# Kernel tuning notes

Measured on AMD Instinct MI355X. Metric: run time of the kernel, lower is better.

Reference implementation:

```python
import jax, jax.numpy as jnp
import numpy as np

D_MODEL = 1024
NUM_HEADS = 16
D_HEAD = D_MODEL // NUM_HEADS


def rotate_half(x):
    half = x.shape[-1] // 2
    x1, x2 = x[..., :half], x[..., half:]
    return jnp.concatenate((-x2, x1), axis=-1)


def rope_cos_sin(seq_len, d_head, dtype):
    # inv_freq over even dims of d_head
    inv_freq = 1.0 / (10000.0 ** (jnp.arange(0, d_head, 2, dtype=jnp.float32) / d_head))
    t = jnp.arange(seq_len, dtype=jnp.float32)
    freqs = jnp.einsum('i,j->ij', t, inv_freq)        # [L, d_head/2]
    emb = jnp.concatenate((freqs, freqs), axis=-1)    # [L, d_head]
    return jnp.cos(emb).astype(dtype), jnp.sin(emb).astype(dtype)


def setup_inputs() -> dict:
    key = jax.random.key(0)
    ks = jax.random.split(key, 9)
    B, L = 2, 2048
    s = 1.0 / np.sqrt(D_MODEL)
    return {
        'x': jax.random.normal(ks[0], (B, L, D_MODEL), dtype=jnp.float32),
        'Wq': jax.random.normal(ks[1], (D_MODEL, D_MODEL), dtype=jnp.float32) * s,
        'bq': jax.random.normal(ks[2], (D_MODEL,), dtype=jnp.float32) * 0.02,
        'Wk': jax.random.normal(ks[3], (D_MODEL, D_MODEL), dtype=jnp.float32) * s,
        'bk': jax.random.normal(ks[4], (D_MODEL,), dtype=jnp.float32) * 0.02,
        'Wv': jax.random.normal(ks[5], (D_MODEL, D_MODEL), dtype=jnp.float32) * s,
        'bv': jax.random.normal(ks[6], (D_MODEL,), dtype=jnp.float32) * 0.02,
        'Wo': jax.random.normal(ks[7], (D_MODEL, D_MODEL), dtype=jnp.float32) * s,
        'bo': jax.random.normal(ks[8], (D_MODEL,), dtype=jnp.float32) * 0.02,
    }


def reference(x, Wq, bq, Wk, bk, Wv, bv, Wo, bo):
    B, L, D = x.shape
    H, Dh = NUM_HEADS, D_HEAD
    scale = Dh ** -0.5

    # projections: torch Linear is x @ W.T + b; here W stored as [in, out]-like
    # square matrices, so treat Wq etc. directly as x @ Wq + bq.
    q = (x @ Wq + bq).reshape(B, L, H, Dh).transpose(0, 2, 1, 3)  # [B,H,L,Dh]
    k = (x @ Wk + bk).reshape(B, L, H, Dh).transpose(0, 2, 1, 3)
    v = (x @ Wv + bv).reshape(B, L, H, Dh).transpose(0, 2, 1, 3)

    cos, sin = rope_cos_sin(L, Dh, x.dtype)  # [L, Dh]
    cos = cos[None, None]  # [1,1,L,Dh]
    sin = sin[None, None]
    q = q * cos + rotate_half(q) * sin
    k = k * cos + rotate_half(k) * sin

    attn = jnp.einsum('bhqd,bhkd->bhqk', q, k) * scale  # [B,H,L,L]
    attn = jax.nn.softmax(attn, axis=-1)
    out = jnp.einsum('bhqk,bhkd->bhqd', attn, v)        # [B,H,L,Dh]
    out = out.transpose(0, 2, 1, 3).reshape(B, L, D)
    return out @ Wo + bo
```

## Files before the change

kernel.cpp:

```cpp
#include <hip/hip_runtime.h>
#include <cmath>

#define D_MODEL  1024
#define NHEADS   16
#define DHEAD    64
#define BATCH    2
#define SEQ      2048
#define MROWS    (BATCH * SEQ)
#define HALF_DH  32

typedef __attribute__((ext_vector_type(8))) short short8;
typedef __attribute__((ext_vector_type(4))) float f32x4;
typedef __attribute__((ext_vector_type(16))) float f32x16;

#define MFMA16(A,B,C) __builtin_amdgcn_mfma_f32_16x16x32_bf16(A,B,C,0,0,0)
#define MFMA32(A,B,C) __builtin_amdgcn_mfma_f32_32x32x16_bf16(A,B,C,0,0,0)

__device__ __forceinline__ unsigned short f2bf(float f) {
    unsigned int u = __float_as_uint(f);
    u += 0x7fffu + ((u >> 16) & 1u);
    return (unsigned short)(u >> 16);
}

__device__ __forceinline__ void gload_lds16(const void* g, void* l) {
    __builtin_amdgcn_global_load_lds(
        (const __attribute__((address_space(1))) unsigned int*)g,
        (__attribute__((address_space(3))) unsigned int*)l,
        16, 0, 0);
}

__global__ void rope_table_kernel(float* __restrict__ cosT, float* __restrict__ sinT) {
    int idx = blockIdx.x * blockDim.x + threadIdx.x;
    if (idx >= SEQ * HALF_DH) return;
    int l = idx >> 5;
    int j = idx & 31;
    float inv = powf(10000.0f, -(float)(2 * j) / (float)DHEAD);
    float ang = (float)l * inv;
    cosT[idx] = cosf(ang);
    sinT[idx] = sinf(ang);
}

__global__ __launch_bounds__(256)
void convert_bf16_kernel(const float* __restrict__ in, unsigned short* __restrict__ out) {
    int i = blockIdx.x * 256 + threadIdx.x;
    float4 v = ((const float4*)in)[i];
    ushort4 o;
    o.x = f2bf(v.x); o.y = f2bf(v.y); o.z = f2bf(v.z); o.w = f2bf(v.w);
    ((ushort4*)out)[i] = o;
}

__global__ __launch_bounds__(256)
void wtrans_kernel(const float* __restrict__ W, unsigned short* __restrict__ Wt) {
    __shared__ unsigned short T[64][68];
    const int k0 = blockIdx.x * 64, n0 = blockIdx.y * 64;
    const int t = threadIdx.x, r = t >> 4, cq = t & 15;
    #pragma unroll
    for (int p = 0; p < 4; ++p) {
        int k = r + 16 * p;
        float4 v = *(const float4*)&W[(size_t)(k0 + k) * D_MODEL + n0 + cq * 4];
        T[cq * 4 + 0][k] = f2bf(v.x);
        T[cq * 4 + 1][k] = f2bf(v.y);
        T[cq * 4 + 2][k] = f2bf(v.z);
        T[cq * 4 + 3][k] = f2bf(v.w);
    }
    __syncthreads();
    #pragma unroll
    for (int p = 0; p < 4; ++p) {
        int n = r + 16 * p;
        ushort4 o;
        o.x = T[n][cq * 4 + 0]; o.y = T[n][cq * 4 + 1];
        o.z = T[n][cq * 4 + 2]; o.w = T[n][cq * 4 + 3];
        *(ushort4*)&Wt[(size_t)(n0 + n) * D_MODEL + k0 + cq * 4] = o;
    }
}

template<int MODE>
__global__ __launch_bounds__(256)
void proj_mfma_kernel(const unsigned short* __restrict__ A, const unsigned short* __restrict__ Bt,
                      const float* __restrict__ bias, const float* __restrict__ cosT,
                      const float* __restrict__ sinT, void* __restrict__ outp)
{
    __shared__ unsigned short As[128 * 64];
    __shared__ unsigned short Bs[64 * 64];
    const int tid = threadIdx.x;
    const int w = tid >> 6, ln = tid & 63;
    const int c = ln & 15, g = ln >> 4;
    const int bm = blockIdx.x * 128, bn = blockIdx.y * 64;
    const int srow = ln >> 3, sblk = ln & 7;

    f32x4 acc[2][4];
    #pragma unroll
    for (int mi = 0; mi < 2; ++mi)
        #pragma unroll
        for (int ni = 0; ni < 4; ++ni) acc[mi][ni] = (f32x4){0.f, 0.f, 0.f, 0.f};

    for (int k0 = 0; k0 < D_MODEL; k0 += 64) {
        __syncthreads();
        #pragma unroll
        for (int i = 0; i < 4; ++i) {
            int chunk = w * 4 + i;
            int row = chunk * 8 + srow;
            int gcol = (sblk ^ (row & 7)) * 8;
            gload_lds16(&A[(size_t)(bm + row) * D_MODEL + k0 + gcol], &As[chunk * 512]);
        }
        #pragma unroll
        for (int i = 0; i < 2; ++i) {
            int chunk = w * 2 + i;
            int row = chunk * 8 + srow;
            int gcol = (sblk ^ (row & 7)) * 8;
            gload_lds16(&Bt[(size_t)(bn + row) * D_MODEL + k0 + gcol], &Bs[chunk * 512]);
        }
        __syncthreads();

        #pragma unroll
        for (int ks = 0; ks < 2; ++ks) {
            const int koff = (ks * 32 + g * 8) ^ ((c & 7) * 8);
            short8 af[2];
            #pragma unroll
            for (int mi = 0; mi < 2; ++mi)
                af[mi] = *(const short8*)&As[(w * 32 + mi * 16 + c) * 64 + koff];
            #pragma unroll
            for (int ni = 0; ni < 4; ++ni) {
                short8 bfr = *(const short8*)&Bs[(ni * 16 + c) * 64 + koff];
                #pragma unroll
                for (int mi = 0; mi < 2; ++mi)
                    acc[mi][ni] = MFMA16(af[mi], bfr, acc[mi][ni]);
            }
        }
    }

    float bv[4];
    #pragma unroll
    for (int ni = 0; ni < 4; ++ni) bv[ni] = bias[bn + ni * 16 + c];

    #pragma unroll
    for (int mi = 0; mi < 2; ++mi) {
        #pragma unroll
        for (int r = 0; r < 4; ++r) {
            const int m = bm + w * 32 + mi * 16 + g * 4 + r;
            float v[4];
            #pragma unroll
            for (int ni = 0; ni < 4; ++ni) v[ni] = acc[mi][ni][r] + bv[ni];
            if (MODE == 2) {
                float* out = (float*)outp;
                #pragma unroll
                for (int ni = 0; ni < 4; ++ni)
                    out[(size_t)m * D_MODEL + bn + ni * 16 + c] = v[ni];
            } else {
                const int b = m >> 11, ll = m & (SEQ - 1);
                if (MODE == 0) {
                    #pragma unroll
                    for (int ni = 0; ni < 2; ++ni) {
                        int d = ni * 16 + c;
                        float co = cosT[ll * HALF_DH + d];
                        float si = sinT[ll * HALF_DH + d];
                        float lo = v[ni], hi = v[ni + 2];
                        v[ni]     = lo * co - hi * si;
                        v[ni + 2] = hi * co + lo * si;
                    }
                }
                const int h = blockIdx.y;
                unsigned short* dst = (unsigned short*)outp
                    + ((size_t)(b * NHEADS + h) * SEQ + ll) * DHEAD;
                #pragma unroll
                for (int ni = 0; ni < 4; ++ni) dst[ni * 16 + c] = f2bf(v[ni]);
            }
        }
    }
}

__global__ __launch_bounds__(256)
void vtrans_kernel(const unsigned short* __restrict__ V, unsigned short* __restrict__ Vt) {
    __shared__ unsigned short T[64][68];
    const int bh = blockIdx.y, l0 = blockIdx.x * 64;
    const int t = threadIdx.x, r = t >> 4, cq = t & 15;
    const unsigned short* Vb = V + (size_t)bh * SEQ * DHEAD;
    #pragma unroll
    for (int p = 0; p < 4; ++p) {
        int ll = r + 16 * p;
        ushort4 v = *(const ushort4*)&Vb[(size_t)(l0 + ll) * DHEAD + cq * 4];
        T[cq * 4 + 0][ll] = v.x; T[cq * 4 + 1][ll] = v.y;
        T[cq * 4 + 2][ll] = v.z; T[cq * 4 + 3][ll] = v.w;
    }
    __syncthreads();
    unsigned short* Vo = Vt + (size_t)bh * DHEAD * SEQ;
    #pragma unroll
    for (int p = 0; p < 4; ++p) {
        int d = r + 16 * p;
        ushort4 o;
        o.x = T[d][cq * 4 + 0]; o.y = T[d][cq * 4 + 1];
        o.z = T[d][cq * 4 + 2]; o.w = T[d][cq * 4 + 3];
        *(ushort4*)&Vo[(size_t)d * SEQ + l0 + cq * 4] = o;
    }
}

__global__ __launch_bounds__(256, 2)
void attn_mfma32_kernel(const unsigned short* __restrict__ Q, const unsigned short* __restrict__ K,
                        const unsigned short* __restrict__ Vt, unsigned short* __restrict__ O)
{
    __shared__ unsigned short Ks[2][64 * 64];
    __shared__ unsigned short Vs[2][64 * 64];
    const int tid = threadIdx.x;
    const int w = tid >> 6, ln = tid & 63;
    const int ql = ln & 31;
    const int h  = ln >> 5;
    const int bh = blockIdx.y;
    const int q  = blockIdx.x * 128 + w * 32 + ql;
    const float SC = 0.125f * 1.44269504088896340736f;
    const int srow = ln >> 3, sblk = ln & 7;

    const unsigned short* Qb = Q  + (size_t)bh * SEQ * DHEAD;
    const unsigned short* Kb = K  + (size_t)bh * SEQ * DHEAD;
    const unsigned short* Vb = Vt + (size_t)bh * DHEAD * SEQ;

    short8 qf[4];
    #pragma unroll
    for (int dk = 0; dk < 4; ++dk)
        qf[dk] = *(const short8*)&Qb[(size_t)q * DHEAD + dk * 16 + h * 8];

    f32x16 accO0, accO1;
    #pragma unroll
    for (int r = 0; r < 16; ++r) { accO0[r] = 0.f; accO1[r] = 0.f; }
    float accL = 0.f, mst = -1e30f;

    #pragma unroll
    for (int i = 0; i < 2; ++i) {
        int chunk = w * 2 + i;
        int row = chunk * 8 + srow;
        int gcol = (sblk ^ (row & 7)) * 8;
        gload_lds16(&Kb[(size_t)row * DHEAD + gcol], &Ks[0][chunk * 512]);
        gload_lds16(&Vb[(size_t)row * SEQ + gcol],   &Vs[0][chunk * 512]);
    }
    __syncthreads();

    int cur = 0;
    for (int kt = 0; kt < SEQ; kt += 64) {
        if (kt + 64 < SEQ) {
            #pragma unroll
            for (int i = 0; i < 2; ++i) {
                int chunk = w * 2 + i;
                int row = chunk * 8 + srow;
                int gcol = (sblk ^ (row & 7)) * 8;
                gload_lds16(&Kb[(size_t)(kt + 64 + row) * DHEAD + gcol], &Ks[cur ^ 1][chunk * 512]);
                gload_lds16(&Vb[(size_t)row * SEQ + kt + 64 + gcol],     &Vs[cur ^ 1][chunk * 512]);
            }
        }

        f32x16 s0, s1;
        #pragma unroll
        for (int r = 0; r < 16; ++r) { s0[r] = 0.f; s1[r] = 0.f; }
        #pragma unroll
        for (int dk = 0; dk < 4; ++dk) {
            const int off = ((2 * dk + h) ^ (ql & 7)) * 8;
            short8 kf0 = *(const short8*)&Ks[cur][ql * 64 + off];
            short8 kf1 = *(const short8*)&Ks[cur][(32 + ql) * 64 + off];
            s0 = MFMA32(kf0, qf[dk], s0);
            s1 = MFMA32(kf1, qf[dk], s1);
        }

        float mx = s0[0];
        #pragma unroll
        for (int r = 1; r < 16; ++r) mx = fmaxf(mx, s0[r]);
        #pragma unroll
        for (int r = 0; r < 16; ++r) mx = fmaxf(mx, s1[r]);
        mx = fmaxf(mx, __shfl_xor(mx, 32));
        const float mn = fmaxf(mst, mx);
        const float rsc = exp2f((mst - mn) * SC);
        mst = mn;

        #pragma unroll
        for (int r = 0; r < 16; ++r) {
            s0[r] = exp2f((s0[r] - mn) * SC);
            s1[r] = exp2f((s1[r] - mn) * SC);
        }

        float ts = 0.f;
        #pragma unroll
        for (int r = 0; r < 16; ++r) ts += s0[r] + s1[r];
        ts += __shfl_xor(ts, 32);
        accL = accL * rsc + ts;

        #pragma unroll
        for (int r = 0; r < 16; ++r) { accO0[r] *= rsc; accO1[r] *= rsc; }

        short8 pf[4];
        #define REPACK_T(T, SV)                                                          \
        {                                                                                \
            unsigned int wA0, wA1, wB0, wB1;                                             \
            asm("v_cvt_pk_bf16_f32 %0, %1, %2" : "=v"(wA0)                               \
                : "v"((SV)[8 * ((T) & 1) + 0]), "v"((SV)[8 * ((T) & 1) + 1]));           \
            asm("v_cvt_pk_bf16_f32 %0, %1, %2" : "=v"(wA1)                               \
                : "v"((SV)[8 * ((T) & 1) + 2]), "v"((SV)[8 * ((T) & 1) + 3]));           \
            asm("v_cvt_pk_bf16_f32 %0, %1, %2" : "=v"(wB0)                               \
                : "v"((SV)[8 * ((T) & 1) + 4]), "v"((SV)[8 * ((T) & 1) + 5]));           \
            asm("v_cvt_pk_bf16_f32 %0, %1, %2" : "=v"(wB1)                               \
                : "v"((SV)[8 * ((T) & 1) + 6]), "v"((SV)[8 * ((T) & 1) + 7]));           \
            asm("v_permlane32_swap_b32 %0, %1" : "+v"(wA0), "+v"(wB0));                  \
            asm("v_permlane32_swap_b32 %0, %1" : "+v"(wA1), "+v"(wB1));                  \
            union { short8 v; unsigned int u[4]; } tmp;                                  \
            tmp.u[0] = wA0; tmp.u[1] = wA1; tmp.u[2] = wB0; tmp.u[3] = wB1;              \
            pf[T] = tmp.v;                                                               \
        }
        REPACK_T(0, s0) REPACK_T(1, s0) REPACK_T(2, s1) REPACK_T(3, s1)
        #undef REPACK_T

        #pragma unroll
        for (int t = 0; t < 4; ++t) {
            const int off = ((2 * t + h) ^ (ql & 7)) * 8;
            short8 vf0 = *(const short8*)&Vs[cur][ql * 64 + off];
            short8 vf1 = *(const short8*)&Vs[cur][(32 + ql) * 64 + off];
            accO0 = MFMA32(vf0, pf[t], accO0);
            accO1 = MFMA32(vf1, pf[t], accO1);
        }

        __syncthreads();
        cur ^= 1;
    }

    const int b = bh >> 4, hh = bh & 15;
    const float inv = 1.0f / accL;
    unsigned short* dst = O + ((size_t)(b * SEQ + q)) * D_MODEL + hh * DHEAD;
    #define EPI(ACC, DC)                                                                 \
    {                                                                                    \
        _Pragma("unroll")                                                                \
        for (int rq = 0; rq < 4; ++rq) {                                                 \
            float a0 = (ACC)[4 * rq + 0] * inv, a1 = (ACC)[4 * rq + 1] * inv;            \
            float a2 = (ACC)[4 * rq + 2] * inv, a3 = (ACC)[4 * rq + 3] * inv;            \
            unsigned int p0, p1;                                                         \
            asm("v_cvt_pk_bf16_f32 %0, %1, %2" : "=v"(p0) : "v"(a0), "v"(a1));           \
            asm("v_cvt_pk_bf16_f32 %0, %1, %2" : "=v"(p1) : "v"(a2), "v"(a3));           \
            uint2 pk; pk.x = p0; pk.y = p1;                                              \
            *(uint2*)(dst + 32 * (DC) + 8 * rq + 4 * h) = pk;                            \
        }                                                                                \
    }
    EPI(accO0, 0) EPI(accO1, 1)
    #undef EPI
}

extern "C" void kernel_launch(void* const* d_in, const int* in_sizes, int n_in,
                              void* d_out, int out_size, void* d_ws, size_t ws_size,
                              hipStream_t stream)
{
    const float* x  = (const float*)d_in[0];
    const float* Wq = (const float*)d_in[1];
    const float* bq = (const float*)d_in[2];
    const float* Wk = (const float*)d_in[3];
    const float* bk = (const float*)d_in[4];
    const float* Wv = (const float*)d_in[5];
    const float* bv = (const float*)d_in[6];
    const float* Wo = (const float*)d_in[7];
    const float* bo = (const float*)d_in[8];

    float* cosT = (float*)d_ws;
    float* sinT = cosT + SEQ * HALF_DH;
    unsigned short* xb  = (unsigned short*)(sinT + SEQ * HALF_DH);
    unsigned short* wqT = xb  + (size_t)MROWS * D_MODEL;
    unsigned short* wkT = wqT + (size_t)D_MODEL * D_MODEL;
    unsigned short* wvT = wkT + (size_t)D_MODEL * D_MODEL;
    unsigned short* woT = wvT + (size_t)D_MODEL * D_MODEL;
    unsigned short* qb  = woT + (size_t)D_MODEL * D_MODEL;
    unsigned short* kb  = qb  + (size_t)MROWS * D_MODEL;
    unsigned short* vb  = kb  + (size_t)MROWS * D_MODEL;
    unsigned short* vtb = vb  + (size_t)MROWS * D_MODEL;
    unsigned short* ob  = vtb + (size_t)MROWS * D_MODEL;

    rope_table_kernel<<<(SEQ * HALF_DH + 255) / 256, 256, 0, stream>>>(cosT, sinT);
    convert_bf16_kernel<<<(MROWS * D_MODEL / 4) / 256, 256, 0, stream>>>(x, xb);

    dim3 wgrid(D_MODEL / 64, D_MODEL / 64);
    wtrans_kernel<<<wgrid, 256, 0, stream>>>(Wq, wqT);
    wtrans_kernel<<<wgrid, 256, 0, stream>>>(Wk, wkT);
    wtrans_kernel<<<wgrid, 256, 0, stream>>>(Wv, wvT);
    wtrans_kernel<<<wgrid, 256, 0, stream>>>(Wo, woT);

    dim3 pgrid(MROWS / 128, D_MODEL / 64);
    proj_mfma_kernel<0><<<pgrid, 256, 0, stream>>>(xb, wqT, bq, cosT, sinT, qb);
    proj_mfma_kernel<0><<<pgrid, 256, 0, stream>>>(xb, wkT, bk, cosT, sinT, kb);
    proj_mfma_kernel<1><<<pgrid, 256, 0, stream>>>(xb, wvT, bv, cosT, sinT, vb);

    dim3 vgrid(SEQ / 64, BATCH * NHEADS);
    vtrans_kernel<<<vgrid, 256, 0, stream>>>(vb, vtb);

    dim3 agrid(SEQ / 128, BATCH * NHEADS);
    attn_mfma32_kernel<<<agrid, 256, 0, stream>>>(qb, kb, vtb, ob);

    proj_mfma_kernel<2><<<pgrid, 256, 0, stream>>>(ob, woT, bo, cosT, sinT, d_out);
}
```

Baseline: 168.5 us.

## Fuse QKV projections with V transpose, split-K attention, lazy softmax rescale

Merges the four weight-transpose launches into one and the three QKV projection launches into one grid-z kernel. The V projection now writes its transposed layout directly through LDS, which removes the separate vtrans pass. Attention is split along the key dimension into two halves to double the grid, with a combine kernel merging the partial results. The online softmax now skips rescaling when the running max does not change, uses tree reductions, and raises the occupancy hint. This costs extra fp32 partial-result traffic and an additional launch for the combine step.

```diff
diff --git a/kernel.cpp b/kernel.cpp
--- a/kernel.cpp
+++ b/kernel.cpp
@@ -8,6 +8,8 @@
 #define SEQ      2048
 #define MROWS    (BATCH * SEQ)
 #define HALF_DH  32
+#define BHTOT    (BATCH * NHEADS)
+#define QROWS    (BHTOT * SEQ)
 
 typedef __attribute__((ext_vector_type(8))) short short8;
 typedef __attribute__((ext_vector_type(4))) float f32x4;
@@ -50,35 +52,164 @@
 }
 
 __global__ __launch_bounds__(256)
-void wtrans_kernel(const float* __restrict__ W, unsigned short* __restrict__ Wt) {
+void wtrans4_kernel(const float* __restrict__ Wq, const float* __restrict__ Wk,
+                    const float* __restrict__ Wv, const float* __restrict__ Wo,
+                    unsigned short* __restrict__ q, unsigned short* __restrict__ k,
+                    unsigned short* __restrict__ v, unsigned short* __restrict__ o)
+{
     __shared__ unsigned short T[64][68];
+    const float* W; unsigned short* Wt;
+    switch (blockIdx.z) {
+        case 0:  W = Wq; Wt = q; break;
+        case 1:  W = Wk; Wt = k; break;
+        case 2:  W = Wv; Wt = v; break;
+        default: W = Wo; Wt = o; break;
+    }
     const int k0 = blockIdx.x * 64, n0 = blockIdx.y * 64;
     const int t = threadIdx.x, r = t >> 4, cq = t & 15;
     #pragma unroll
     for (int p = 0; p < 4; ++p) {
-        int k = r + 16 * p;
-        float4 v = *(const float4*)&W[(size_t)(k0 + k) * D_MODEL + n0 + cq * 4];
-        T[cq * 4 + 0][k] = f2bf(v.x);
-        T[cq * 4 + 1][k] = f2bf(v.y);
-        T[cq * 4 + 2][k] = f2bf(v.z);
-        T[cq * 4 + 3][k] = f2bf(v.w);
+        int kk = r + 16 * p;
+        float4 vv = *(const float4*)&W[(size_t)(k0 + kk) * D_MODEL + n0 + cq * 4];
+        T[cq * 4 + 0][kk] = f2bf(vv.x);
+        T[cq * 4 + 1][kk] = f2bf(vv.y);
+        T[cq * 4 + 2][kk] = f2bf(vv.z);
+        T[cq * 4 + 3][kk] = f2bf(vv.w);
     }
     __syncthreads();
     #pragma unroll
     for (int p = 0; p < 4; ++p) {
         int n = r + 16 * p;
-        ushort4 o;
-        o.x = T[n][cq * 4 + 0]; o.y = T[n][cq * 4 + 1];
-        o.z = T[n][cq * 4 + 2]; o.w = T[n][cq * 4 + 3];
-        *(ushort4*)&Wt[(size_t)(n0 + n) * D_MODEL + k0 + cq * 4] = o;
-    }
-}
-
-template<int MODE>
+        ushort4 ov;
+        ov.x = T[n][cq * 4 + 0]; ov.y = T[n][cq * 4 + 1];
+        ov.z = T[n][cq * 4 + 2]; ov.w = T[n][cq * 4 + 3];
+        *(ushort4*)&Wt[(size_t)(n0 + n) * D_MODEL + k0 + cq * 4] = ov;
+    }
+}
+
 __global__ __launch_bounds__(256)
-void proj_mfma_kernel(const unsigned short* __restrict__ A, const unsigned short* __restrict__ Bt,
-                      const float* __restrict__ bias, const float* __restrict__ cosT,
-                      const float* __restrict__ sinT, void* __restrict__ outp)
+void qkv_proj_kernel(const unsigned short* __restrict__ A,
+                     const unsigned short* __restrict__ wqT, const unsigned short* __restrict__ wkT,
+                     const unsigned short* __restrict__ wvT,
+                     const float* __restrict__ bq, const float* __restrict__ bk,
+                     const float* __restrict__ bv,
+                     const float* __restrict__ cosT, const float* __restrict__ sinT,
+                     unsigned short* __restrict__ qb, unsigned short* __restrict__ kb,
+                     unsigned short* __restrict__ vtb)
+{
+    __shared__ unsigned short SMEM[128 * 64 + 64 * 64];
+    unsigned short* As = SMEM;
+    unsigned short* Bs = SMEM + 128 * 64;
+
+    const int z = blockIdx.z;
+    const unsigned short* Bt = (z == 0) ? wqT : (z == 1) ? wkT : wvT;
+    const float* bias = (z == 0) ? bq : (z == 1) ? bk : bv;
+
+    const int tid = threadIdx.x;
+    const int w = tid >> 6, ln = tid & 63;
+    const int c = ln & 15, g = ln >> 4;
+    const int bm = blockIdx.x * 128, bn = blockIdx.y * 64;
+    const int srow = ln >> 3, sblk = ln & 7;
+
+    f32x4 acc[2][4];
+    #pragma unroll
+    for (int mi = 0; mi < 2; ++mi)
+        #pragma unroll
+        for (int ni = 0; ni < 4; ++ni) acc[mi][ni] = (f32x4){0.f, 0.f, 0.f, 0.f};
+
+    for (int k0 = 0; k0 < D_MODEL; k0 += 64) {
+        __syncthreads();
+        #pragma unroll
+        for (int i = 0; i < 4; ++i) {
+            int chunk = w * 4 + i;
+            int row = chunk * 8 + srow;
+            int gcol = (sblk ^ (row & 7)) * 8;
+            gload_lds16(&A[(size_t)(bm + row) * D_MODEL + k0 + gcol], &As[chunk * 512]);
+        }
+        #pragma unroll
+        for (int i = 0; i < 2; ++i) {
+            int chunk = w * 2 + i;
+            int row = chunk * 8 + srow;
+            int gcol = (sblk ^ (row & 7)) * 8;
+            gload_lds16(&Bt[(size_t)(bn + row) * D_MODEL + k0 + gcol], &Bs[chunk * 512]);
+        }
+        __syncthreads();
+
+        #pragma unroll
+        for (int ks = 0; ks < 2; ++ks) {
+            const int koff = (ks * 32 + g * 8) ^ ((c & 7) * 8);
+            short8 af[2];
+            #pragma unroll
+            for (int mi = 0; mi < 2; ++mi)
+                af[mi] = *(const short8*)&As[(w * 32 + mi * 16 + c) * 64 + koff];
+            #pragma unroll
+            for (int ni = 0; ni < 4; ++ni) {
+                short8 bfr = *(const short8*)&Bs[(ni * 16 + c) * 64 + koff];
+                #pragma unroll
+                for (int mi = 0; mi < 2; ++mi)
+                    acc[mi][ni] = MFMA16(af[mi], bfr, acc[mi][ni]);
+            }
+        }
+    }
+
+    float bv4[4];
+    #pragma unroll
+    for (int ni = 0; ni < 4; ++ni) bv4[ni] = bias[bn + ni * 16 + c];
+
+    if (z < 2) {
+        unsigned short* op = z ? kb : qb;
+        const int hy = blockIdx.y;
+        #pragma unroll
+        for (int mi = 0; mi < 2; ++mi) {
+            #pragma unroll
+            for (int r = 0; r < 4; ++r) {
+                const int m = bm + w * 32 + mi * 16 + g * 4 + r;
+                const int b = m >> 11, ll = m & (SEQ - 1);
+                float v[4];
+                #pragma unroll
+                for (int ni = 0; ni < 4; ++ni) v[ni] = acc[mi][ni][r] + bv4[ni];
+                #pragma unroll
+                for (int ni = 0; ni < 2; ++ni) {
+                    int d = ni * 16 + c;
+                    float co = cosT[ll * HALF_DH + d];
+                    float si = sinT[ll * HALF_DH + d];
+                    float lo = v[ni], hi = v[ni + 2];
+                    v[ni]     = lo * co - hi * si;
+                    v[ni + 2] = hi * co + lo * si;
+                }
+                unsigned short* dst = op + ((size_t)(b * NHEADS + hy) * SEQ + ll) * DHEAD;
+                #pragma unroll
+                for (int ni = 0; ni < 4; ++ni) dst[ni * 16 + c] = f2bf(v[ni]);
+            }
+        }
+    } else {
+        unsigned short (*T)[136] = (unsigned short(*)[136])SMEM;
+        __syncthreads();
+        #pragma unroll
+        for (int mi = 0; mi < 2; ++mi)
+            #pragma unroll
+            for (int r = 0; r < 4; ++r)
+                #pragma unroll
+                for (int ni = 0; ni < 4; ++ni)
+                    T[ni * 16 + c][w * 32 + mi * 16 + g * 4 + r] = f2bf(acc[mi][ni][r] + bv4[ni]);
+        __syncthreads();
+        const int b  = bm >> 11;
+        const int l0 = bm & (SEQ - 1);
+        const int bh = b * NHEADS + blockIdx.y;
+        unsigned short* Vo = vtb + (size_t)bh * DHEAD * SEQ;
+        #pragma unroll
+        for (int it = 0; it < 4; ++it) {
+            int row  = (tid >> 4) + it * 16;
+            int col8 = tid & 15;
+            uint4 val = *(const uint4*)&T[row][col8 * 8];
+            *(uint4*)&Vo[(size_t)row * SEQ + l0 + col8 * 8] = val;
+        }
+    }
+}
+
+__global__ __launch_bounds__(256)
+void outproj_kernel(const unsigned short* __restrict__ A, const unsigned short* __restrict__ Bt,
+                    const float* __restrict__ bias, float* __restrict__ out)
 {
     __shared__ unsigned short As[128 * 64];
     __shared__ unsigned short Bs[64 * 64];
@@ -129,74 +260,24 @@
         }
     }
 
-    float bv[4];
-    #pragma unroll
-    for (int ni = 0; ni < 4; ++ni) bv[ni] = bias[bn + ni * 16 + c];
-
-    #pragma unroll
-    for (int mi = 0; mi < 2; ++mi) {
+    float bv4[4];
+    #pragma unroll
+    for (int ni = 0; ni < 4; ++ni) bv4[ni] = bias[bn + ni * 16 + c];
+    #pragma unroll
+    for (int mi = 0; mi < 2; ++mi)
         #pragma unroll
         for (int r = 0; r < 4; ++r) {
             const int m = bm + w * 32 + mi * 16 + g * 4 + r;
-            float v[4];
-            #pragma unroll
-            for (int ni = 0; ni < 4; ++ni) v[ni] = acc[mi][ni][r] + bv[ni];
-            if (MODE == 2) {
-                float* out = (float*)outp;
-                #pragma unroll
-                for (int ni = 0; ni < 4; ++ni)
-                    out[(size_t)m * D_MODEL + bn + ni * 16 + c] = v[ni];
-            } else {
-                const int b = m >> 11, ll = m & (SEQ - 1);
-                if (MODE == 0) {
-                    #pragma unroll
-                    for (int ni = 0; ni < 2; ++ni) {
-                        int d = ni * 16 + c;
-                        float co = cosT[ll * HALF_DH + d];
-                        float si = sinT[ll * HALF_DH + d];
-                        float lo = v[ni], hi = v[ni + 2];
-                        v[ni]     = lo * co - hi * si;
-                        v[ni + 2] = hi * co + lo * si;
-                    }
-                }
-                const int h = blockIdx.y;
-                unsigned short* dst = (unsigned short*)outp
-                    + ((size_t)(b * NHEADS + h) * SEQ + ll) * DHEAD;
-                #pragma unroll
-                for (int ni = 0; ni < 4; ++ni) dst[ni * 16 + c] = f2bf(v[ni]);
-            }
-        }
-    }
-}
-
-__global__ __launch_bounds__(256)
-void vtrans_kernel(const unsigned short* __restrict__ V, unsigned short* __restrict__ Vt) {
-    __shared__ unsigned short T[64][68];
-    const int bh = blockIdx.y, l0 = blockIdx.x * 64;
-    const int t = threadIdx.x, r = t >> 4, cq = t & 15;
-    const unsigned short* Vb = V + (size_t)bh * SEQ * DHEAD;
-    #pragma unroll
-    for (int p = 0; p < 4; ++p) {
-        int ll = r + 16 * p;
-        ushort4 v = *(const ushort4*)&Vb[(size_t)(l0 + ll) * DHEAD + cq * 4];
-        T[cq * 4 + 0][ll] = v.x; T[cq * 4 + 1][ll] = v.y;
-        T[cq * 4 + 2][ll] = v.z; T[cq * 4 + 3][ll] = v.w;
-    }
-    __syncthreads();
-    unsigned short* Vo = Vt + (size_t)bh * DHEAD * SEQ;
-    #pragma unroll
-    for (int p = 0; p < 4; ++p) {
-        int d = r + 16 * p;
-        ushort4 o;
-        o.x = T[d][cq * 4 + 0]; o.y = T[d][cq * 4 + 1];
-        o.z = T[d][cq * 4 + 2]; o.w = T[d][cq * 4 + 3];
-        *(ushort4*)&Vo[(size_t)d * SEQ + l0 + cq * 4] = o;
-    }
-}
-
-__global__ __launch_bounds__(256, 2)
+            #pragma unroll
+            for (int ni = 0; ni < 4; ++ni)
+                out[(size_t)m * D_MODEL + bn + ni * 16 + c] = acc[mi][ni][r] + bv4[ni];
+        }
+}
+
+__global__ __launch_bounds__(256, 4)
 void attn_mfma32_kernel(const unsigned short* __restrict__ Q, const unsigned short* __restrict__ K,
-                        const unsigned short* __restrict__ Vt, unsigned short* __restrict__ O)
+                        const unsigned short* __restrict__ Vt, unsigned short* __restrict__ O,
+                        float* __restrict__ accP, float* __restrict__ ml, int nsplit)
 {
     __shared__ unsigned short Ks[2][64 * 64];
     __shared__ unsigned short Vs[2][64 * 64];
@@ -206,6 +287,9 @@
     const int h  = ln >> 5;
     const int bh = blockIdx.y;
     const int q  = blockIdx.x * 128 + w * 32 + ql;
+    const int split = blockIdx.z;
+    const int ntile = SEQ / (64 * nsplit);
+    const int kt0 = split * (SEQ / nsplit);
     const float SC = 0.125f * 1.44269504088896340736f;
     const int srow = ln >> 3, sblk = ln & 7;
 
@@ -228,14 +312,15 @@
         int chunk = w * 2 + i;
         int row = chunk * 8 + srow;
         int gcol = (sblk ^ (row & 7)) * 8;
-        gload_lds16(&Kb[(size_t)row * DHEAD + gcol], &Ks[0][chunk * 512]);
-        gload_lds16(&Vb[(size_t)row * SEQ + gcol],   &Vs[0][chunk * 512]);
+        gload_lds16(&Kb[(size_t)(kt0 + row) * DHEAD + gcol], &Ks[0][chunk * 512]);
+        gload_lds16(&Vb[(size_t)row * SEQ + kt0 + gcol],     &Vs[0][chunk * 512]);
     }
     __syncthreads();
 
     int cur = 0;
-    for (int kt = 0; kt < SEQ; kt += 64) {
-        if (kt + 64 < SEQ) {
+    for (int it = 0; it < ntile; ++it) {
+        const int kt = kt0 + it * 64;
+        if (it + 1 < ntile) {
             #pragma unroll
             for (int i = 0; i < 2; ++i) {
                 int chunk = w * 2 + i;
@@ -258,30 +343,41 @@
             s1 = MFMA32(kf1, qf[dk], s1);
         }
 
-        float mx = s0[0];
-        #pragma unroll
-        for (int r = 1; r < 16; ++r) mx = fmaxf(mx, s0[r]);
-        #pragma unroll
-        for (int r = 0; r < 16; ++r) mx = fmaxf(mx, s1[r]);
+        float m16[16];
+        #pragma unroll
+        for (int r = 0; r < 16; ++r) m16[r] = fmaxf(s0[r], s1[r]);
+        #pragma unroll
+        for (int st = 8; st >= 1; st >>= 1)
+            #pragma unroll
+            for (int r = 0; r < st; ++r) m16[r] = fmaxf(m16[r], m16[r + st]);
+        float mx = m16[0];
         mx = fmaxf(mx, __shfl_xor(mx, 32));
+
         const float mn = fmaxf(mst, mx);
-        const float rsc = exp2f((mst - mn) * SC);
-        mst = mn;
+        if (__any(mn > mst)) {
+            const float rsc = exp2f((mst - mn) * SC);
+            #pragma unroll
+            for (int r = 0; r < 16; ++r) { accO0[r] *= rsc; accO1[r] *= rsc; }
+            accL *= rsc;
+            mst = mn;
+        }
 
         #pragma unroll
         for (int r = 0; r < 16; ++r) {
-            s0[r] = exp2f((s0[r] - mn) * SC);
-            s1[r] = exp2f((s1[r] - mn) * SC);
-        }
-
-        float ts = 0.f;
-        #pragma unroll
-        for (int r = 0; r < 16; ++r) ts += s0[r] + s1[r];
+            s0[r] = exp2f((s0[r] - mst) * SC);
+            s1[r] = exp2f((s1[r] - mst) * SC);
+        }
+
+        float t16[16];
+        #pragma unroll
+        for (int r = 0; r < 16; ++r) t16[r] = s0[r] + s1[r];
+        #pragma unroll
+        for (int st = 8; st >= 1; st >>= 1)
+            #pragma unroll
+            for (int r = 0; r < st; ++r) t16[r] += t16[r + st];
+        float ts = t16[0];
         ts += __shfl_xor(ts, 32);
-        accL = accL * rsc + ts;
-
-        #pragma unroll
-        for (int r = 0; r < 16; ++r) { accO0[r] *= rsc; accO1[r] *= rsc; }
+        accL += ts;
 
         short8 pf[4];
         #define REPACK_T(T, SV)                                                          \
@@ -317,24 +413,70 @@
         cur ^= 1;
     }
 
-    const int b = bh >> 4, hh = bh & 15;
-    const float inv = 1.0f / accL;
-    unsigned short* dst = O + ((size_t)(b * SEQ + q)) * D_MODEL + hh * DHEAD;
-    #define EPI(ACC, DC)                                                                 \
-    {                                                                                    \
-        _Pragma("unroll")                                                                \
-        for (int rq = 0; rq < 4; ++rq) {                                                 \
-            float a0 = (ACC)[4 * rq + 0] * inv, a1 = (ACC)[4 * rq + 1] * inv;            \
-            float a2 = (ACC)[4 * rq + 2] * inv, a3 = (ACC)[4 * rq + 3] * inv;            \
-            unsigned int p0, p1;                                                         \
-            asm("v_cvt_pk_bf16_f32 %0, %1, %2" : "=v"(p0) : "v"(a0), "v"(a1));           \
-            asm("v_cvt_pk_bf16_f32 %0, %1, %2" : "=v"(p1) : "v"(a2), "v"(a3));           \
-            uint2 pk; pk.x = p0; pk.y = p1;                                              \
-            *(uint2*)(dst + 32 * (DC) + 8 * rq + 4 * h) = pk;                            \
-        }                                                                                \
-    }
-    EPI(accO0, 0) EPI(accO1, 1)
-    #undef EPI
+    if (nsplit == 1) {
+        const int b = bh >> 4, hh = bh & 15;
+        const float inv = 1.0f / accL;
+        unsigned short* dst = O + ((size_t)(b * SEQ + q)) * D_MODEL + hh * DHEAD;
+        #define EPI(ACC, DC)                                                             \
+        {                                                                                \
+            _Pragma("unroll")                                                            \
+            for (int rq = 0; rq < 4; ++rq) {                                             \
+                float a0 = (ACC)[4 * rq + 0] * inv, a1 = (ACC)[4 * rq + 1] * inv;        \
+                float a2 = (ACC)[4 * rq + 2] * inv, a3 = (ACC)[4 * rq + 3] * inv;        \
+                unsigned int p0, p1;                                                     \
+                asm("v_cvt_pk_bf16_f32 %0, %1, %2" : "=v"(p0) : "v"(a0), "v"(a1));       \
+                asm("v_cvt_pk_bf16_f32 %0, %1, %2" : "=v"(p1) : "v"(a2), "v"(a3));       \
+                uint2 pk; pk.x = p0; pk.y = p1;                                          \
+                *(uint2*)(dst + 32 * (DC) + 8 * rq + 4 * h) = pk;                        \
+            }                                                                            \
+        }
+        EPI(accO0, 0) EPI(accO1, 1)
+        #undef EPI
+    } else {
+        float* base = accP + ((size_t)(split * BHTOT + bh) * SEQ + q) * 64;
+        #pragma unroll
+        for (int rq = 0; rq < 4; ++rq) {
+            float4 v0, v1;
+            v0.x = accO0[4 * rq + 0]; v0.y = accO0[4 * rq + 1];
+            v0.z = accO0[4 * rq + 2]; v0.w = accO0[4 * rq + 3];
+            v1.x = accO1[4 * rq + 0]; v1.y = accO1[4 * rq + 1];
+            v1.z = accO1[4 * rq + 2]; v1.w = accO1[4 * rq + 3];
+            *(float4*)&base[8 * rq + 4 * h]      = v0;
+            *(float4*)&base[32 + 8 * rq + 4 * h] = v1;
+        }
+        if (h == 0) {
+            float2 v; v.x = mst; v.y = accL;
+            ((float2*)ml)[(size_t)(split * BHTOT + bh) * SEQ + q] = v;
+        }
+    }
+}
+
+__global__ __launch_bounds__(256)
+void combine2_kernel(const float* __restrict__ accP, const float* __restrict__ ml,
+                     unsigned short* __restrict__ ob)
+{
+    const float SC = 0.125f * 1.44269504088896340736f;
+    int t = blockIdx.x * 256 + threadIdx.x;
+    int d4  = (t & 15) * 4;
+    int bhq = t >> 4;
+    const float2* ML = (const float2*)ml;
+    float2 m0 = ML[bhq];
+    float2 m1 = ML[(size_t)QROWS + bhq];
+    float M  = fmaxf(m0.x, m1.x);
+    float w0 = exp2f((m0.x - M) * SC);
+    float w1 = exp2f((m1.x - M) * SC);
+    float inv = 1.0f / (w0 * m0.y + w1 * m1.y);
+    float4 a0 = *(const float4*)&accP[(size_t)bhq * 64 + d4];
+    float4 a1 = *(const float4*)&accP[(size_t)QROWS * 64 + (size_t)bhq * 64 + d4];
+    float o0 = (a0.x * w0 + a1.x * w1) * inv;
+    float o1 = (a0.y * w0 + a1.y * w1) * inv;
+    float o2 = (a0.z * w0 + a1.z * w1) * inv;
+    float o3 = (a0.w * w0 + a1.w * w1) * inv;
+    int bh = bhq >> 11, q = bhq & (SEQ - 1);
+    int b = bh >> 4, hh = bh & 15;
+    ushort4 ov;
+    ov.x = f2bf(o0); ov.y = f2bf(o1); ov.z = f2bf(o2); ov.w = f2bf(o3);
+    *(ushort4*)&ob[((size_t)(b * SEQ + q)) * D_MODEL + hh * DHEAD + d4] = ov;
 }
 
 extern "C" void kernel_launch(void* const* d_in, const int* in_sizes, int n_in,
@@ -351,38 +493,37 @@
     const float* Wo = (const float*)d_in[7];
     const float* bo = (const float*)d_in[8];
 
-    float* cosT = (float*)d_ws;
-    float* sinT = cosT + SEQ * HALF_DH;
-    unsigned short* xb  = (unsigned short*)(sinT + SEQ * HALF_DH);
-    unsigned short* wqT = xb  + (size_t)MROWS * D_MODEL;
-    unsigned short* wkT = wqT + (size_t)D_MODEL * D_MODEL;
-    unsigned short* wvT = wkT + (size_t)D_MODEL * D_MODEL;
-    unsigned short* woT = wvT + (size_t)D_MODEL * D_MODEL;
-    unsigned short* qb  = woT + (size_t)D_MODEL * D_MODEL;
-    unsigned short* kb  = qb  + (size_t)MROWS * D_MODEL;
-    unsigned short* vb  = kb  + (size_t)MROWS * D_MODEL;
-    unsigned short* vtb = vb  + (size_t)MROWS * D_MODEL;
-    unsigned short* ob  = vtb + (size_t)MROWS * D_MODEL;
+    char* p = (char*)d_ws;
+    float* cosT = (float*)p;            p += (size_t)SEQ * HALF_DH * 4;
+    float* sinT = (float*)p;            p += (size_t)SEQ * HALF_DH * 4;
+    unsigned short* xb  = (unsigned short*)p; p += (size_t)MROWS * D_MODEL * 2;
+    unsigned short* wqT = (unsigned short*)p; p += (size_t)D_MODEL * D_MODEL * 2;
+    unsigned short* wkT = (unsigned short*)p; p += (size_t)D_MODEL * D_MODEL * 2;
+    unsigned short* wvT = (unsigned short*)p; p += (size_t)D_MODEL * D_MODEL * 2;
+    unsigned short* woT = (unsigned short*)p; p += (size_t)D_MODEL * D_MODEL * 2;
+    unsigned short* qb  = (unsigned short*)p; p += (size_t)MROWS * D_MODEL * 2;
+    unsigned short* kb  = (unsigned short*)p; p += (size_t)MROWS * D_MODEL * 2;
+    unsigned short* vtb = (unsigned short*)p; p += (size_t)MROWS * D_MODEL * 2;
+    unsigned short* ob  = (unsigned short*)p; p += (size_t)MROWS * D_MODEL * 2;
+    float* accP = (float*)p;            p += (size_t)2 * QROWS * 64 * 4;
+    float* ml   = (float*)p;            p += (size_t)2 * QROWS * 2 * 4;
+    size_t need2 = (size_t)(p - (char*)d_ws);
+    const int nsplit = (ws_size >= need2) ? 2 : 1;
 
     rope_table_kernel<<<(SEQ * HALF_DH + 255) / 256, 256, 0, stream>>>(cosT, sinT);
     convert_bf16_kernel<<<(MROWS * D_MODEL / 4) / 256, 256, 0, stream>>>(x, xb);
 
-    dim3 wgrid(D_MODEL / 64, D_MODEL / 64);
-    wtrans_kernel<<<wgrid, 256, 0, stream>>>(Wq, wqT);
-    wtrans_kernel<<<wgrid, 256, 0, stream>>>(Wk, wkT);
-    wtrans_kernel<<<wgrid, 256, 0, stream>>>(Wv, wvT);
-    wtrans_kernel<<<wgrid, 256, 0, stream>>>(Wo, woT);
-
-    dim3 pgrid(MROWS / 128, D_MODEL / 64);
-    proj_mfma_kernel<0><<<pgrid, 256, 0, stream>>>(xb, wqT, bq, cosT, sinT, qb);
-    proj_mfma_kernel<0><<<pgrid, 256, 0, stream>>>(xb, wkT, bk, cosT, sinT, kb);
-    proj_mfma_kernel<1><<<pgrid, 256, 0, stream>>>(xb, wvT, bv, cosT, sinT, vb);
-
-    dim3 vgrid(SEQ / 64, BATCH * NHEADS);
-    vtrans_kernel<<<vgrid, 256, 0, stream>>>(vb, vtb);
-
-    dim3 agrid(SEQ / 128, BATCH * NHEADS);
-    attn_mfma32_kernel<<<agrid, 256, 0, stream>>>(qb, kb, vtb, ob);
-
-    proj_mfma_kernel<2><<<pgrid, 256, 0, stream>>>(ob, woT, bo, cosT, sinT, d_out);
-}
+    wtrans4_kernel<<<dim3(D_MODEL / 64, D_MODEL / 64, 4), 256, 0, stream>>>(
+        Wq, Wk, Wv, Wo, wqT, wkT, wvT, woT);
+
+    qkv_proj_kernel<<<dim3(MROWS / 128, D_MODEL / 64, 3), 256, 0, stream>>>(
+        xb, wqT, wkT, wvT, bq, bk, bv, cosT, sinT, qb, kb, vtb);
+
+    attn_mfma32_kernel<<<dim3(SEQ / 128, BHTOT, nsplit), 256, 0, stream>>>(
+        qb, kb, vtb, ob, accP, ml, nsplit);
+
+    if (nsplit == 2)
+        combine2_kernel<<<(QROWS * 16) / 256, 256, 0, stream>>>(accP, ml, ob);
+
+    outproj_kernel<<<dim3(MROWS / 128, D_MODEL / 64), 256, 0, stream>>>(ob, woT, bo, (float*)d_out);
+}
```

Result: faster. 152.6 us (-9.4%).
